# Kernel tuning notes

Hardware: AMD Instinct MI355X
Metric: run time of the kernel (lower is better)

The kernel has to match this reference:

```python
import jax, jax.numpy as jnp
import numpy as np

B, E, H, DEPTH = 8192, 512, 512, 1


def setup_inputs() -> dict:
    key = jax.random.key(0)
    ks = jax.random.split(key, 10)
    inp = {
        "X": jax.random.normal(ks[0], (B, E), jnp.float32),
        "prev_a": jax.random.normal(ks[1], (B, DEPTH + 1, H), jnp.float32),
        "prev_b": jax.random.normal(ks[2], (B, DEPTH + 1, H), jnp.float32),
        "prev_depth": jax.random.randint(ks[3], (B, 1), 0, DEPTH + 1, jnp.int32),
        # torch.nn.Linear weights, shape [out, in], y = x @ W.T
        "w_f": jax.random.normal(ks[4], (1, H), jnp.float32) * 0.02,
        "w_a00": jax.random.normal(ks[5], (H, E + H), jnp.float32) * 0.02,
        "w_a10": jax.random.normal(ks[6], (H, E + H), jnp.float32) * 0.02,
        "w_b00": jax.random.normal(ks[7], (H, E + 2 * H), jnp.float32) * 0.02,
        "w_b11": jax.random.normal(ks[8], (H, E + H), jnp.float32) * 0.02,
        "w_b10": jax.random.normal(ks[9], (H, E + H), jnp.float32) * 0.02,
    }
    return inp


def reference(X, prev_a, prev_b, prev_depth, w_f, w_a00, w_a10, w_b00, w_b11, w_b10):
    dt = X.dtype
    # gather prev_b at current depth per batch row: prev_b[b, prev_depth[b,0], :]
    b_top = jnp.take_along_axis(prev_b, prev_depth[:, :, None], axis=1)[:, 0, :]  # [B,H]
    # fork decision; torch rounds then casts to long -> no grad flows through w_f
    f_raw = jax.lax.stop_gradient(jnp.round(jax.nn.sigmoid(b_top @ w_f.T)))  # [B,1]
    all_zero = jnp.all(prev_depth == 0)
    f = jnp.where(all_zero, jnp.ones_like(f_raw), f_raw)
    j = jnp.where(all_zero, jnp.zeros_like(f_raw), f_raw)  # else-branch sets j = f
    next_depth = prev_depth + (f - j).astype(prev_depth.dtype)  # [B,1]

    d = 1  # depth fixed to 1
    pa, pb0, pb1 = prev_a[:, d, :], prev_b[:, d - 1, :], prev_b[:, d, :]

    fj, nn_, fn = f * j, (1.0 - f) * (1.0 - j), f * (1.0 - j)  # [B,1] gates
    eq = (next_depth == d).astype(dt)
    lt = (next_depth < d).astype(dt)

    nofork_nojoin_a = jnp.concatenate([X, pa], 1) @ w_a00.T
    fork_nojoin_a = jnp.concatenate([X, pb0], 1) @ w_a10.T
    next_a1 = eq * (fj * pa + nn_ * nofork_nojoin_a + fn * fork_nojoin_a) + lt * pa

    fork_join_b = jnp.concatenate([X, pb1], 1) @ w_b11.T
    nofork_nojoin_b = jnp.concatenate([X, pa, next_a1], 1) @ w_b00.T
    fork_nojoin_b = jnp.concatenate([X, next_a1], 1) @ w_b10.T
    next_b1 = eq * (fj * fork_join_b + nn_ * nofork_nojoin_b + fn * fork_nojoin_b) + lt * pb1

    zeros = jnp.zeros_like(next_a1)
    next_a = jnp.stack([zeros, next_a1], 1)  # [B, 2, H]
    next_b = jnp.stack([zeros, next_b1], 1)  # [B, 2, H]
    return next_a, next_b, next_depth, f, j
```

## Files before the change

kernel.cpp:

```cpp
#include <hip/hip_runtime.h>
#include <hip/hip_bf16.h>

typedef __attribute__((ext_vector_type(8))) __bf16 bf16x8;
typedef __attribute__((ext_vector_type(4))) float f32x4;
typedef __attribute__((ext_vector_type(4))) unsigned short u16x4;
typedef unsigned short u16;
typedef unsigned long long u64;

typedef __attribute__((address_space(1))) void gvoid;
typedef __attribute__((address_space(3))) void lvoid;

#define B_DIM 8192
#define MFMA(a, b, c) __builtin_amdgcn_mfma_f32_16x16x32_bf16((a), (b), (c), 0, 0, 0)

__device__ __forceinline__ u16x4 cvt4(f32x4 v) {
    u16x4 r;
    r.x = __builtin_bit_cast(u16, __float2bfloat16(v.x));
    r.y = __builtin_bit_cast(u16, __float2bfloat16(v.y));
    r.z = __builtin_bit_cast(u16, __float2bfloat16(v.z));
    r.w = __builtin_bit_cast(u16, __float2bfloat16(v.w));
    return r;
}

__device__ __forceinline__ void stage64(const u16* g, int ldg, u16* ls, int t) {
#pragma unroll
    for (int it = 0; it < 2; ++it) {
        int e = it * 2048 + t * 8;
        int r = e >> 6;
        int slot = (e & 63) >> 3;
        int csrc = (slot ^ (r & 7)) << 3;
        __builtin_amdgcn_global_load_lds((gvoid*)(g + (size_t)r * ldg + csrc),
                                         (lvoid*)&ls[e], 16, 0, 0);
    }
}

__device__ __forceinline__ bf16x8 ld_frag(const u16* ls, int row, int kslot) {
    return *(const bf16x8*)&ls[row * 64 + ((kslot ^ (row & 7)) << 3)];
}

__global__ void k_pre(const float* __restrict__ X, const float* __restrict__ prev_a,
                      const float* __restrict__ prev_b, const int* __restrict__ prev_depth,
                      const float* __restrict__ w_f,
                      const float* __restrict__ wa00f, const float* __restrict__ wa10f,
                      const float* __restrict__ wb00f, const float* __restrict__ wb11f,
                      const float* __restrict__ wb10f,
                      u16* __restrict__ Xb, u16* __restrict__ pab,
                      u16* __restrict__ pb0b, u16* __restrict__ pb1b,
                      u16* __restrict__ wa00b, u16* __restrict__ wa10b,
                      u16* __restrict__ wb00b, u16* __restrict__ wb11b,
                      u16* __restrict__ wb10b,
                      float* __restrict__ dotv,
                      float* __restrict__ outA, float* __restrict__ outB) {
    int blk = blockIdx.x;
    if (blk >= 2048) {
        int t = (blk - 2048) * 256 + threadIdx.x;
        const int S = 131072, SB = 196608;
        const float* src; u16* dst; int off;
        if      (t < S)            { src = wa00f; dst = wa00b; off = t; }
        else if (t < 2 * S)        { src = wa10f; dst = wa10b; off = t - S; }
        else if (t < 2 * S + SB)   { src = wb00f; dst = wb00b; off = t - 2 * S; }
        else if (t < 3 * S + SB)   { src = wb11f; dst = wb11b; off = t - 2 * S - SB; }
        else if (t < 4 * S + SB)   { src = wb10f; dst = wb10b; off = t - 3 * S - SB; }
        else return;
        f32x4 v = *(const f32x4*)(src + (size_t)off * 4);
        *(u16x4*)(dst + (size_t)off * 4) = cvt4(v);
        return;
    }
    int wv = threadIdx.x >> 6, l = threadIdx.x & 63;
    int row = blk * 4 + wv;
    size_t r512 = (size_t)row * 512, r1024 = (size_t)row * 1024;
    const int i1 = l * 4;
    const int i2 = 256 + l * 4;
    f32x4 x0  = *(const f32x4*)(X + r512 + i1);
    f32x4 x1  = *(const f32x4*)(X + r512 + i2);
    f32x4 pa0 = *(const f32x4*)(prev_a + r1024 + 512 + i1);
    f32x4 pa1 = *(const f32x4*)(prev_a + r1024 + 512 + i2);
    f32x4 q00 = *(const f32x4*)(prev_b + r1024 + i1);
    f32x4 q01 = *(const f32x4*)(prev_b + r1024 + i2);
    f32x4 q10 = *(const f32x4*)(prev_b + r1024 + 512 + i1);
    f32x4 q11 = *(const f32x4*)(prev_b + r1024 + 512 + i2);
    f32x4 w0  = *(const f32x4*)(w_f + i1);
    f32x4 w1  = *(const f32x4*)(w_f + i2);
    int depth = prev_depth[row];
    f32x4 b0 = depth ? q10 : q00;
    f32x4 b1 = depth ? q11 : q01;
    float dot = b0.x*w0.x + b0.y*w0.y + b0.z*w0.z + b0.w*w0.w
              + b1.x*w1.x + b1.y*w1.y + b1.z*w1.z + b1.w*w1.w;
    for (int off = 32; off > 0; off >>= 1) dot += __shfl_xor(dot, off, 64);

    *(u16x4*)(Xb   + r512 + i1) = cvt4(x0);
    *(u16x4*)(Xb   + r512 + i2) = cvt4(x1);
    *(u16x4*)(pab  + r512 + i1) = cvt4(pa0);
    *(u16x4*)(pab  + r512 + i2) = cvt4(pa1);
    *(u16x4*)(pb0b + r512 + i1) = cvt4(q00);
    *(u16x4*)(pb0b + r512 + i2) = cvt4(q01);
    *(u16x4*)(pb1b + r512 + i1) = cvt4(q10);
    *(u16x4*)(pb1b + r512 + i2) = cvt4(q11);
    f32x4 z; z.x = 0.f; z.y = 0.f; z.z = 0.f; z.w = 0.f;
    *(f32x4*)(outA + r1024 + i1) = z;
    *(f32x4*)(outA + r1024 + i2) = z;
    *(f32x4*)(outB + r1024 + i1) = z;
    *(f32x4*)(outB + r1024 + i2) = z;
    if (l == 0) dotv[row] = dot;
}

__global__ __launch_bounds__(1024) void k_scan(
        const float* __restrict__ dotv, const int* __restrict__ prev_depth,
        int* __restrict__ info, int* __restrict__ idx, int* __restrict__ cnt) {
    __shared__ u64 wtot[16];
    __shared__ int wany[16];
    const int tid = threadIdx.x, lane = tid & 63, wv = tid >> 6;
    int r0 = tid * 8;
    int dep[8]; float dv[8];
    int any = 0;
#pragma unroll
    for (int r = 0; r < 8; ++r) {
        dep[r] = prev_depth[r0 + r];
        dv[r] = dotv[r0 + r];
        any |= dep[r];
    }
    for (int off = 32; off > 0; off >>= 1) any |= __shfl_xor(any, off, 64);
    if (lane == 0) wany[wv] = any;
    __syncthreads();
    int ga = 0;
#pragma unroll
    for (int w = 0; w < 16; ++w) ga |= wany[w];
    int az = (ga == 0);

    int rcls[8], rf[8], rj[8], rnd[8];
    u64 pk = 0;
#pragma unroll
    for (int r = 0; r < 8; ++r) {
        float sg = 1.0f / (1.0f + expf(-dv[r]));
        int fi = (int)rintf(sg);
        int f = az ? 1 : fi;
        int j = az ? 0 : fi;
        int nd = dep[r] + f - j;
        int cls;
        if (nd == 1)     cls = f ? (j ? 2 : 1) : 0;
        else             cls = (nd < 1) ? 3 : 4;
        rcls[r] = cls; rf[r] = f; rj[r] = j; rnd[r] = nd;
        if (cls < 3) pk += 1ull << (cls * 21);
    }
    u64 own = pk;
    for (int off = 1; off < 64; off <<= 1) {
        u64 v = __shfl_up(pk, off, 64);
        if (lane >= off) pk += v;
    }
    if (lane == 63) wtot[wv] = pk;
    __syncthreads();
    u64 wbase = 0, tot = 0;
#pragma unroll
    for (int w = 0; w < 16; ++w) {
        u64 v = wtot[w];
        if (w < wv) wbase += v;
        tot += v;
    }
    u64 excl = wbase + pk - own;
    const u64 M21 = (1ull << 21) - 1;
    int tot0 = (int)(tot & M21), tot1 = (int)((tot >> 21) & M21), tot2 = (int)((tot >> 42) & M21);
    int base0 = 0;
    int base1 = (tot0 + 63) & ~63;
    int base2 = base1 + ((tot1 + 63) & ~63);
    int o0 = base0 + (int)(excl & M21);
    int o1 = base1 + (int)((excl >> 21) & M21);
    int o2 = base2 + (int)((excl >> 42) & M21);
#pragma unroll
    for (int r = 0; r < 8; ++r) {
        int row = r0 + r, cls = rcls[r], pos = 0;
        if (cls == 0)      { pos = o0++; idx[pos] = row; }
        else if (cls == 1) { pos = o1++; idx[pos] = row; }
        else if (cls == 2) { pos = o2++; idx[pos] = row; }
        info[row] = cls | (rf[r] << 3) | (rj[r] << 4) | (rnd[r] << 5) | (pos << 7);
    }
    if (tid < 64) {
        int p0 = tot0 + tid;          if (p0 < base1) idx[p0] = 0;
        int p1 = base1 + tot1 + tid;  if (p1 < base2) idx[p1] = 0;
        int end2 = base2 + ((tot2 + 63) & ~63);
        int p2 = base2 + tot2 + tid;  if (p2 < end2) idx[p2] = 0;
    }
    if (tid == 0) {
        cnt[0] = tot0; cnt[1] = tot1; cnt[2] = tot2;
        cnt[4] = base0; cnt[5] = base1; cnt[6] = base2;
    }
}

__global__ __launch_bounds__(256, 4) void k_s1x(
    const u16* __restrict__ Xb, const u16* __restrict__ pab,
    const u16* __restrict__ pb0b, const u16* __restrict__ pb1b,
    const u16* __restrict__ wa00, const u16* __restrict__ wa10,
    const u16* __restrict__ wb00, const u16* __restrict__ wb11,
    const u16* __restrict__ wb10,
    const int* __restrict__ idx, const int* __restrict__ cnt, const int* __restrict__ info,
    const float* __restrict__ prev_a, const float* __restrict__ prev_b,
    u16* __restrict__ na1_all, float* __restrict__ part,
    float* __restrict__ outA, float* __restrict__ outB,
    float* __restrict__ outD, float* __restrict__ outF, float* __restrict__ outJ)
{
    __shared__ u16 lsA[4096], lsB0[4096], lsB1[4096];
    int blk = (int)blockIdx.x;
    if (blk >= 1040) {
        int pb_ = blk - 1040;
        int wv = threadIdx.x >> 6, l = threadIdx.x & 63;
        int row = pb_ * 4 + wv;
        int inf = info[row];
        int cls = inf & 7;
        size_t r1024 = (size_t)row * 1024;
        const int i1 = l * 4, i2 = 256 + l * 4;
        if (l == 0) {
            outD[row] = (float)((inf >> 5) & 3);
            outF[row] = (float)((inf >> 3) & 1);
            outJ[row] = (float)((inf >> 4) & 1);
        }
        if (cls == 2 || cls == 3) {
            f32x4 pa0 = *(const f32x4*)(prev_a + r1024 + 512 + i1);
            f32x4 pa1 = *(const f32x4*)(prev_a + r1024 + 512 + i2);
            *(f32x4*)(outA + r1024 + 512 + i1) = pa0;
            *(f32x4*)(outA + r1024 + 512 + i2) = pa1;
            if (cls == 3) {
                f32x4 q10 = *(const f32x4*)(prev_b + r1024 + 512 + i1);
                f32x4 q11 = *(const f32x4*)(prev_b + r1024 + 512 + i2);
                *(f32x4*)(outB + r1024 + 512 + i1) = q10;
                *(f32x4*)(outB + r1024 + 512 + i2) = q11;
            }
        } else if (cls == 4) {
            f32x4 z; z.x = 0.f; z.y = 0.f; z.z = 0.f; z.w = 0.f;
            *(f32x4*)(outA + r1024 + 512 + i1) = z;
            *(f32x4*)(outA + r1024 + 512 + i2) = z;
            *(f32x4*)(outB + r1024 + 512 + i1) = z;
            *(f32x4*)(outB + r1024 + 512 + i2) = z;
        }
        return;
    }
    int c0 = cnt[0], c1 = cnt[1], c2 = cnt[2];
    int base0 = cnt[4], base1 = cnt[5], base2 = cnt[6];
    int t0 = (c0 + 63) >> 6, t1 = (c1 + 63) >> 6, t2 = (c2 + 63) >> 6;
    int T = blk >> 3, nt = blk & 7;
    int cls, mb, cc;
    const u16 *W0, *W1 = nullptr, *S2;
    int ldW1 = 0;
    if (T < t0)                { cls = 0; mb = base0 + T * 64; cc = c0; W0 = wa00; W1 = wb00; ldW1 = 1536; S2 = pab; }
    else if (T < t0 + t1)      { T -= t0; cls = 1; mb = base1 + T * 64; cc = c1; W0 = wa10; W1 = wb10; ldW1 = 1024; S2 = pb0b; }
    else if (T < t0 + t1 + t2) { T -= t0 + t1; cls = 2; mb = base2 + T * 64; cc = c2; W0 = wb11; S2 = pb1b; }
    else return;
    const int t = threadIdx.x;
    const int n0 = nt * 64;
    const int lane = t & 63, wv = t >> 6;
    const int wr = (wv >> 1) * 32, wc = (wv & 1) * 32;
    const int fr = lane & 15, fq = lane >> 4;

    int ri0 = idx[mb + (t >> 3)];
    int ri1 = idx[mb + 32 + (t >> 3)];
    const u16* xg0 = Xb + (size_t)ri0 * 512;
    const u16* xg1 = Xb + (size_t)ri1 * 512;
    const u16* sg0 = S2 + (size_t)ri0 * 512;
    const u16* sg1 = S2 + (size_t)ri1 * 512;
    const int csrc = ((t & 7) ^ ((t >> 3) & 7)) << 3;

    f32x4 acc0[2][2] = {}, acc1[2][2] = {};

    for (int kq = 0; kq < 16; ++kq) {
        int cb = (kq & 7) * 64;
        const u16* a0 = (kq < 8) ? xg0 : sg0;
        const u16* a1 = (kq < 8) ? xg1 : sg1;
        __builtin_amdgcn_global_load_lds((gvoid*)(a0 + cb + csrc), (lvoid*)&lsA[t * 8], 16, 0, 0);
        __builtin_amdgcn_global_load_lds((gvoid*)(a1 + cb + csrc), (lvoid*)&lsA[2048 + t * 8], 16, 0, 0);
        stage64(W0 + (size_t)n0 * 1024 + kq * 64, 1024, lsB0, t);
        bool dual = (cls == 0) || (cls == 1 && kq < 8);
        if (dual) stage64(W1 + (size_t)n0 * ldW1 + kq * 64, ldW1, lsB1, t);
        __syncthreads();
#pragma unroll
        for (int kk = 0; kk < 2; ++kk) {
            int ks = kk * 4 + fq;
            bf16x8 a[2], b0[2], b1[2];
#pragma unroll
            for (int mi = 0; mi < 2; ++mi) a[mi] = ld_frag(lsA, wr + mi * 16 + fr, ks);
#pragma unroll
            for (int ni = 0; ni < 2; ++ni) b0[ni] = ld_frag(lsB0, wc + ni * 16 + fr, ks);
            if (dual) {
#pragma unroll
                for (int ni = 0; ni < 2; ++ni) b1[ni] = ld_frag(lsB1, wc + ni * 16 + fr, ks);
            }
#pragma unroll
            for (int mi = 0; mi < 2; ++mi)
#pragma unroll
                for (int ni = 0; ni < 2; ++ni) {
                    acc0[mi][ni] = MFMA(a[mi], b0[ni], acc0[mi][ni]);
                    if (dual) acc1[mi][ni] = MFMA(a[mi], b1[ni], acc1[mi][ni]);
                }
        }
        __syncthreads();
    }
    int lt0 = T * 64;
#pragma unroll
    for (int mi = 0; mi < 2; ++mi)
#pragma unroll
        for (int jj = 0; jj < 4; ++jj) {
            int lr = wr + mi * 16 + fq * 4 + jj;
            if (lt0 + lr >= cc) continue;
            int grow = idx[mb + lr];
#pragma unroll
            for (int ni = 0; ni < 2; ++ni) {
                int col = n0 + wc + ni * 16 + fr;
                float v = acc0[mi][ni][jj];
                if (cls < 2) {
                    na1_all[(size_t)(mb + lr) * 512 + col] = __builtin_bit_cast(u16, __float2bfloat16(v));
                    outA[(size_t)grow * 1024 + 512 + col] = v;
                    part[(size_t)(mb + lr) * 512 + col] = acc1[mi][ni][jj];
                } else {
                    outB[(size_t)grow * 1024 + 512 + col] = v;
                }
            }
        }
}

__global__ __launch_bounds__(256, 4) void k_s2(
    const u16* __restrict__ na1_all,
    const u16* __restrict__ wb00, const u16* __restrict__ wb10,
    const int* __restrict__ idx, const int* __restrict__ cnt,
    const float* __restrict__ part, float* __restrict__ outB)
{
    __shared__ u16 lsA[4096], lsB[4096];
    int c0 = cnt[0], c1 = cnt[1];
    int base0 = cnt[4], base1 = cnt[5];
    int t0 = (c0 + 63) >> 6, t1 = (c1 + 63) >> 6;
    int blk = (int)blockIdx.x;
    int T = blk >> 3, nt = blk & 7;
    int mb, cc, ldW, kofs;
    const u16* W;
    if (T < t0)           { mb = base0 + T * 64; cc = c0; W = wb00; ldW = 1536; kofs = 1024; }
    else if (T < t0 + t1) { T -= t0; mb = base1 + T * 64; cc = c1; W = wb10; ldW = 1024; kofs = 512; }
    else return;
    const int t = threadIdx.x;
    const int n0 = nt * 64;
    const int lane = t & 63, wv = t >> 6;
    const int wr = (wv >> 1) * 32, wc = (wv & 1) * 32;
    const int fr = lane & 15, fq = lane >> 4;

    f32x4 acc[2][2];
#pragma unroll
    for (int mi = 0; mi < 2; ++mi)
#pragma unroll
        for (int ni = 0; ni < 2; ++ni)
#pragma unroll
            for (int jj = 0; jj < 4; ++jj)
                acc[mi][ni][jj] = part[(size_t)(mb + wr + mi * 16 + fq * 4 + jj) * 512
                                       + n0 + wc + ni * 16 + fr];

    for (int kq = 0; kq < 8; ++kq) {
        stage64(na1_all + (size_t)mb * 512 + kq * 64, 512, lsA, t);
        stage64(W + (size_t)n0 * ldW + kofs + kq * 64, ldW, lsB, t);
        __syncthreads();
#pragma unroll
        for (int kk = 0; kk < 2; ++kk) {
            int ks = kk * 4 + fq;
            bf16x8 a[2], b[2];
#pragma unroll
            for (int mi = 0; mi < 2; ++mi) a[mi] = ld_frag(lsA, wr + mi * 16 + fr, ks);
#pragma unroll
            for (int ni = 0; ni < 2; ++ni) b[ni] = ld_frag(lsB, wc + ni * 16 + fr, ks);
#pragma unroll
            for (int mi = 0; mi < 2; ++mi)
#pragma unroll
                for (int ni = 0; ni < 2; ++ni)
                    acc[mi][ni] = MFMA(a[mi], b[ni], acc[mi][ni]);
        }
        __syncthreads();
    }
    int lt0 = T * 64;
#pragma unroll
    for (int mi = 0; mi < 2; ++mi)
#pragma unroll
        for (int jj = 0; jj < 4; ++jj) {
            int lr = wr + mi * 16 + fq * 4 + jj;
            if (lt0 + lr >= cc) continue;
            int grow = idx[mb + lr];
#pragma unroll
            for (int ni = 0; ni < 2; ++ni) {
                int col = n0 + wc + ni * 16 + fr;
                outB[(size_t)grow * 1024 + 512 + col] = acc[mi][ni][jj];
            }
        }
}

extern "C" void kernel_launch(void* const* d_in, const int* in_sizes, int n_in,
                              void* d_out, int out_size, void* d_ws, size_t ws_size,
                              hipStream_t stream) {
    const float* X          = (const float*)d_in[0];
    const float* prev_a     = (const float*)d_in[1];
    const float* prev_b     = (const float*)d_in[2];
    const int*   prev_depth = (const int*)d_in[3];
    const float* w_f        = (const float*)d_in[4];
    const float* w_a00      = (const float*)d_in[5];
    const float* w_a10      = (const float*)d_in[6];
    const float* w_b00      = (const float*)d_in[7];
    const float* w_b11      = (const float*)d_in[8];
    const float* w_b10      = (const float*)d_in[9];

    float* out  = (float*)d_out;
    float* outA = out;
    float* outB = out + 8388608;
    float* outD = out + 16777216;
    float* outF = outD + 8192;
    float* outJ = outF + 8192;

    char* ws = (char*)d_ws;
    size_t off = 0;
    auto alloc = [&](size_t bytes) -> char* {
        char* p = ws + off;
        off += (bytes + 255) & ~(size_t)255;
        return p;
    };
    const int ROWS = 8448;
    u16* Xb     = (u16*)alloc((size_t)B_DIM * 512 * 2);
    u16* pab    = (u16*)alloc((size_t)B_DIM * 512 * 2);
    u16* pb0b   = (u16*)alloc((size_t)B_DIM * 512 * 2);
    u16* pb1b   = (u16*)alloc((size_t)B_DIM * 512 * 2);
    u16* na1_all = (u16*)alloc((size_t)ROWS * 512 * 2);
    float* part  = (float*)alloc((size_t)ROWS * 512 * 4);
    u16* wa00b = (u16*)alloc((size_t)512 * 1024 * 2);
    u16* wa10b = (u16*)alloc((size_t)512 * 1024 * 2);
    u16* wb00b = (u16*)alloc((size_t)512 * 1536 * 2);
    u16* wb11b = (u16*)alloc((size_t)512 * 1024 * 2);
    u16* wb10b = (u16*)alloc((size_t)512 * 1024 * 2);
    float* dotv = (float*)alloc((size_t)B_DIM * 4);
    int* info   = (int*)alloc((size_t)B_DIM * 4);
    int* idx    = (int*)alloc((size_t)ROWS * 4);
    int* cnt    = (int*)alloc(256);
    if (off > ws_size) return;

    k_pre<<<4864, 256, 0, stream>>>(X, prev_a, prev_b, prev_depth, w_f,
                                    w_a00, w_a10, w_b00, w_b11, w_b10,
                                    Xb, pab, pb0b, pb1b,
                                    wa00b, wa10b, wb00b, wb11b, wb10b,
                                    dotv, outA, outB);
    k_scan<<<1, 1024, 0, stream>>>(dotv, prev_depth, info, idx, cnt);
    k_s1x<<<3088, 256, 0, stream>>>(Xb, pab, pb0b, pb1b,
                                    wa00b, wa10b, wb00b, wb11b, wb10b,
                                    idx, cnt, info, prev_a, prev_b,
                                    na1_all, part, outA, outB, outD, outF, outJ);
    k_s2<<<1040, 256, 0, stream>>>(na1_all, wb00b, wb10b, idx, cnt, part, outB);
}
```

Baseline: 68.23 us.

## Gather class-sorted bf16 activation rows after scan instead of converting all inputs upfront

The pre-kernel now only computes the fork dot products from the depth-selected prev_b row and converts the weights. Previously it converted X, pa, pb0 and pb1 for every row. A new mid kernel runs after the scan. It gathers each row's X and its one class-specific second operand into a contiguous, class-sorted bf16 buffer, and it also does the output zeroing and passthrough copies. The GEMM kernel then stages its A tiles with plain contiguous loads instead of indexed row gathers, and it no longer carries the passthrough blocks. This cuts the bf16 conversion traffic and simplifies the GEMM loads, at the cost of one extra kernel launch and a serial dependence between the gather and the GEMM.

```diff
diff --git a/kernel.cpp b/kernel.cpp
--- a/kernel.cpp
+++ b/kernel.cpp
@@ -38,19 +38,15 @@
     return *(const bf16x8*)&ls[row * 64 + ((kslot ^ (row & 7)) << 3)];
 }
 
-__global__ void k_pre(const float* __restrict__ X, const float* __restrict__ prev_a,
-                      const float* __restrict__ prev_b, const int* __restrict__ prev_depth,
-                      const float* __restrict__ w_f,
-                      const float* __restrict__ wa00f, const float* __restrict__ wa10f,
-                      const float* __restrict__ wb00f, const float* __restrict__ wb11f,
-                      const float* __restrict__ wb10f,
-                      u16* __restrict__ Xb, u16* __restrict__ pab,
-                      u16* __restrict__ pb0b, u16* __restrict__ pb1b,
-                      u16* __restrict__ wa00b, u16* __restrict__ wa10b,
-                      u16* __restrict__ wb00b, u16* __restrict__ wb11b,
-                      u16* __restrict__ wb10b,
-                      float* __restrict__ dotv,
-                      float* __restrict__ outA, float* __restrict__ outB) {
+__global__ void k_dots(const float* __restrict__ prev_b, const int* __restrict__ prev_depth,
+                       const float* __restrict__ w_f,
+                       const float* __restrict__ wa00f, const float* __restrict__ wa10f,
+                       const float* __restrict__ wb00f, const float* __restrict__ wb11f,
+                       const float* __restrict__ wb10f,
+                       u16* __restrict__ wa00b, u16* __restrict__ wa10b,
+                       u16* __restrict__ wb00b, u16* __restrict__ wb11b,
+                       u16* __restrict__ wb10b,
+                       float* __restrict__ dotv) {
     int blk = blockIdx.x;
     if (blk >= 2048) {
         int t = (blk - 2048) * 256 + threadIdx.x;
@@ -68,39 +64,16 @@
     }
     int wv = threadIdx.x >> 6, l = threadIdx.x & 63;
     int row = blk * 4 + wv;
-    size_t r512 = (size_t)row * 512, r1024 = (size_t)row * 1024;
-    const int i1 = l * 4;
-    const int i2 = 256 + l * 4;
-    f32x4 x0  = *(const f32x4*)(X + r512 + i1);
-    f32x4 x1  = *(const f32x4*)(X + r512 + i2);
-    f32x4 pa0 = *(const f32x4*)(prev_a + r1024 + 512 + i1);
-    f32x4 pa1 = *(const f32x4*)(prev_a + r1024 + 512 + i2);
-    f32x4 q00 = *(const f32x4*)(prev_b + r1024 + i1);
-    f32x4 q01 = *(const f32x4*)(prev_b + r1024 + i2);
-    f32x4 q10 = *(const f32x4*)(prev_b + r1024 + 512 + i1);
-    f32x4 q11 = *(const f32x4*)(prev_b + r1024 + 512 + i2);
-    f32x4 w0  = *(const f32x4*)(w_f + i1);
-    f32x4 w1  = *(const f32x4*)(w_f + i2);
     int depth = prev_depth[row];
-    f32x4 b0 = depth ? q10 : q00;
-    f32x4 b1 = depth ? q11 : q01;
-    float dot = b0.x*w0.x + b0.y*w0.y + b0.z*w0.z + b0.w*w0.w
-              + b1.x*w1.x + b1.y*w1.y + b1.z*w1.z + b1.w*w1.w;
+    const float* bt = prev_b + (size_t)row * 1024 + (size_t)depth * 512;
+    const int i1 = l * 4, i2 = 256 + l * 4;
+    f32x4 v0 = *(const f32x4*)(bt + i1);
+    f32x4 v1 = *(const f32x4*)(bt + i2);
+    f32x4 w0 = *(const f32x4*)(w_f + i1);
+    f32x4 w1 = *(const f32x4*)(w_f + i2);
+    float dot = v0.x*w0.x + v0.y*w0.y + v0.z*w0.z + v0.w*w0.w
+              + v1.x*w1.x + v1.y*w1.y + v1.z*w1.z + v1.w*w1.w;
     for (int off = 32; off > 0; off >>= 1) dot += __shfl_xor(dot, off, 64);
-
-    *(u16x4*)(Xb   + r512 + i1) = cvt4(x0);
-    *(u16x4*)(Xb   + r512 + i2) = cvt4(x1);
-    *(u16x4*)(pab  + r512 + i1) = cvt4(pa0);
-    *(u16x4*)(pab  + r512 + i2) = cvt4(pa1);
-    *(u16x4*)(pb0b + r512 + i1) = cvt4(q00);
-    *(u16x4*)(pb0b + r512 + i2) = cvt4(q01);
-    *(u16x4*)(pb1b + r512 + i1) = cvt4(q10);
-    *(u16x4*)(pb1b + r512 + i2) = cvt4(q11);
-    f32x4 z; z.x = 0.f; z.y = 0.f; z.z = 0.f; z.w = 0.f;
-    *(f32x4*)(outA + r1024 + i1) = z;
-    *(f32x4*)(outA + r1024 + i2) = z;
-    *(f32x4*)(outB + r1024 + i1) = z;
-    *(f32x4*)(outB + r1024 + i2) = z;
     if (l == 0) dotv[row] = dot;
 }
 
@@ -185,63 +158,92 @@
     }
 }
 
-__global__ __launch_bounds__(256, 4) void k_s1x(
-    const u16* __restrict__ Xb, const u16* __restrict__ pab,
-    const u16* __restrict__ pb0b, const u16* __restrict__ pb1b,
+__global__ void k_mid(const float* __restrict__ X, const float* __restrict__ prev_a,
+                      const float* __restrict__ prev_b,
+                      const int* __restrict__ info, const int* __restrict__ idx,
+                      const int* __restrict__ cnt,
+                      u16* __restrict__ A_all,
+                      float* __restrict__ outA, float* __restrict__ outB,
+                      float* __restrict__ outD, float* __restrict__ outF,
+                      float* __restrict__ outJ) {
+    int blk = (int)blockIdx.x;
+    int wv = threadIdx.x >> 6, l = threadIdx.x & 63;
+    const int i1 = l * 4, i2 = 256 + l * 4;
+    if (blk >= 2048) {
+        int p = (blk - 2048) * 4 + wv;
+        int base1 = cnt[5], base2 = cnt[6];
+        int end2 = base2 + ((cnt[2] + 63) & ~63);
+        if (p >= end2) return;
+        const float* sec = (p < base1) ? (prev_a + 512)
+                         : (p < base2) ? prev_b
+                                       : (prev_b + 512);
+        int row = idx[p];
+        size_t r512 = (size_t)row * 512, r1024 = (size_t)row * 1024;
+        f32x4 xa = *(const f32x4*)(X + r512 + i1);
+        f32x4 xb = *(const f32x4*)(X + r512 + i2);
+        f32x4 sa = *(const f32x4*)(sec + r1024 + i1);
+        f32x4 sb = *(const f32x4*)(sec + r1024 + i2);
+        size_t pbase = (size_t)p * 1024;
+        *(u16x4*)(A_all + pbase + i1)       = cvt4(xa);
+        *(u16x4*)(A_all + pbase + i2)       = cvt4(xb);
+        *(u16x4*)(A_all + pbase + 512 + i1) = cvt4(sa);
+        *(u16x4*)(A_all + pbase + 512 + i2) = cvt4(sb);
+        return;
+    }
+    int row = blk * 4 + wv;
+    int inf = info[row];
+    int cls = inf & 7;
+    size_t r1024 = (size_t)row * 1024;
+    f32x4 z; z.x = 0.f; z.y = 0.f; z.z = 0.f; z.w = 0.f;
+    *(f32x4*)(outA + r1024 + i1) = z;
+    *(f32x4*)(outA + r1024 + i2) = z;
+    *(f32x4*)(outB + r1024 + i1) = z;
+    *(f32x4*)(outB + r1024 + i2) = z;
+    if (l == 0) {
+        outD[row] = (float)((inf >> 5) & 3);
+        outF[row] = (float)((inf >> 3) & 1);
+        outJ[row] = (float)((inf >> 4) & 1);
+    }
+    if (cls == 2 || cls == 3) {
+        f32x4 pa0 = *(const f32x4*)(prev_a + r1024 + 512 + i1);
+        f32x4 pa1 = *(const f32x4*)(prev_a + r1024 + 512 + i2);
+        *(f32x4*)(outA + r1024 + 512 + i1) = pa0;
+        *(f32x4*)(outA + r1024 + 512 + i2) = pa1;
+        if (cls == 3) {
+            f32x4 q10 = *(const f32x4*)(prev_b + r1024 + 512 + i1);
+            f32x4 q11 = *(const f32x4*)(prev_b + r1024 + 512 + i2);
+            *(f32x4*)(outB + r1024 + 512 + i1) = q10;
+            *(f32x4*)(outB + r1024 + 512 + i2) = q11;
+        }
+    } else if (cls == 4) {
+        *(f32x4*)(outA + r1024 + 512 + i1) = z;
+        *(f32x4*)(outA + r1024 + 512 + i2) = z;
+        *(f32x4*)(outB + r1024 + 512 + i1) = z;
+        *(f32x4*)(outB + r1024 + 512 + i2) = z;
+    }
+}
+
+__global__ __launch_bounds__(256, 4) void k_s1(
+    const u16* __restrict__ A_all,
     const u16* __restrict__ wa00, const u16* __restrict__ wa10,
     const u16* __restrict__ wb00, const u16* __restrict__ wb11,
     const u16* __restrict__ wb10,
-    const int* __restrict__ idx, const int* __restrict__ cnt, const int* __restrict__ info,
-    const float* __restrict__ prev_a, const float* __restrict__ prev_b,
+    const int* __restrict__ idx, const int* __restrict__ cnt,
     u16* __restrict__ na1_all, float* __restrict__ part,
-    float* __restrict__ outA, float* __restrict__ outB,
-    float* __restrict__ outD, float* __restrict__ outF, float* __restrict__ outJ)
+    float* __restrict__ outA, float* __restrict__ outB)
 {
     __shared__ u16 lsA[4096], lsB0[4096], lsB1[4096];
-    int blk = (int)blockIdx.x;
-    if (blk >= 1040) {
-        int pb_ = blk - 1040;
-        int wv = threadIdx.x >> 6, l = threadIdx.x & 63;
-        int row = pb_ * 4 + wv;
-        int inf = info[row];
-        int cls = inf & 7;
-        size_t r1024 = (size_t)row * 1024;
-        const int i1 = l * 4, i2 = 256 + l * 4;
-        if (l == 0) {
-            outD[row] = (float)((inf >> 5) & 3);
-            outF[row] = (float)((inf >> 3) & 1);
-            outJ[row] = (float)((inf >> 4) & 1);
-        }
-        if (cls == 2 || cls == 3) {
-            f32x4 pa0 = *(const f32x4*)(prev_a + r1024 + 512 + i1);
-            f32x4 pa1 = *(const f32x4*)(prev_a + r1024 + 512 + i2);
-            *(f32x4*)(outA + r1024 + 512 + i1) = pa0;
-            *(f32x4*)(outA + r1024 + 512 + i2) = pa1;
-            if (cls == 3) {
-                f32x4 q10 = *(const f32x4*)(prev_b + r1024 + 512 + i1);
-                f32x4 q11 = *(const f32x4*)(prev_b + r1024 + 512 + i2);
-                *(f32x4*)(outB + r1024 + 512 + i1) = q10;
-                *(f32x4*)(outB + r1024 + 512 + i2) = q11;
-            }
-        } else if (cls == 4) {
-            f32x4 z; z.x = 0.f; z.y = 0.f; z.z = 0.f; z.w = 0.f;
-            *(f32x4*)(outA + r1024 + 512 + i1) = z;
-            *(f32x4*)(outA + r1024 + 512 + i2) = z;
-            *(f32x4*)(outB + r1024 + 512 + i1) = z;
-            *(f32x4*)(outB + r1024 + 512 + i2) = z;
-        }
-        return;
-    }
     int c0 = cnt[0], c1 = cnt[1], c2 = cnt[2];
     int base0 = cnt[4], base1 = cnt[5], base2 = cnt[6];
     int t0 = (c0 + 63) >> 6, t1 = (c1 + 63) >> 6, t2 = (c2 + 63) >> 6;
+    int blk = (int)blockIdx.x;
     int T = blk >> 3, nt = blk & 7;
     int cls, mb, cc;
-    const u16 *W0, *W1 = nullptr, *S2;
+    const u16 *W0, *W1 = nullptr;
     int ldW1 = 0;
-    if (T < t0)                { cls = 0; mb = base0 + T * 64; cc = c0; W0 = wa00; W1 = wb00; ldW1 = 1536; S2 = pab; }
-    else if (T < t0 + t1)      { T -= t0; cls = 1; mb = base1 + T * 64; cc = c1; W0 = wa10; W1 = wb10; ldW1 = 1024; S2 = pb0b; }
-    else if (T < t0 + t1 + t2) { T -= t0 + t1; cls = 2; mb = base2 + T * 64; cc = c2; W0 = wb11; S2 = pb1b; }
+    if (T < t0)                { cls = 0; mb = base0 + T * 64; cc = c0; W0 = wa00; W1 = wb00; ldW1 = 1536; }
+    else if (T < t0 + t1)      { T -= t0; cls = 1; mb = base1 + T * 64; cc = c1; W0 = wa10; W1 = wb10; ldW1 = 1024; }
+    else if (T < t0 + t1 + t2) { T -= t0 + t1; cls = 2; mb = base2 + T * 64; cc = c2; W0 = wb11; }
     else return;
     const int t = threadIdx.x;
     const int n0 = nt * 64;
@@ -249,25 +251,14 @@
     const int wr = (wv >> 1) * 32, wc = (wv & 1) * 32;
     const int fr = lane & 15, fq = lane >> 4;
 
-    int ri0 = idx[mb + (t >> 3)];
-    int ri1 = idx[mb + 32 + (t >> 3)];
-    const u16* xg0 = Xb + (size_t)ri0 * 512;
-    const u16* xg1 = Xb + (size_t)ri1 * 512;
-    const u16* sg0 = S2 + (size_t)ri0 * 512;
-    const u16* sg1 = S2 + (size_t)ri1 * 512;
-    const int csrc = ((t & 7) ^ ((t >> 3) & 7)) << 3;
-
     f32x4 acc0[2][2] = {}, acc1[2][2] = {};
 
     for (int kq = 0; kq < 16; ++kq) {
-        int cb = (kq & 7) * 64;
-        const u16* a0 = (kq < 8) ? xg0 : sg0;
-        const u16* a1 = (kq < 8) ? xg1 : sg1;
-        __builtin_amdgcn_global_load_lds((gvoid*)(a0 + cb + csrc), (lvoid*)&lsA[t * 8], 16, 0, 0);
-        __builtin_amdgcn_global_load_lds((gvoid*)(a1 + cb + csrc), (lvoid*)&lsA[2048 + t * 8], 16, 0, 0);
-        stage64(W0 + (size_t)n0 * 1024 + kq * 64, 1024, lsB0, t);
+        int cb = kq * 64;
+        stage64(A_all + (size_t)mb * 1024 + cb, 1024, lsA, t);
+        stage64(W0 + (size_t)n0 * 1024 + cb, 1024, lsB0, t);
         bool dual = (cls == 0) || (cls == 1 && kq < 8);
-        if (dual) stage64(W1 + (size_t)n0 * ldW1 + kq * 64, ldW1, lsB1, t);
+        if (dual) stage64(W1 + (size_t)n0 * ldW1 + cb, ldW1, lsB1, t);
         __syncthreads();
 #pragma unroll
         for (int kk = 0; kk < 2; ++kk) {
@@ -412,12 +403,9 @@
         return p;
     };
     const int ROWS = 8448;
-    u16* Xb     = (u16*)alloc((size_t)B_DIM * 512 * 2);
-    u16* pab    = (u16*)alloc((size_t)B_DIM * 512 * 2);
-    u16* pb0b   = (u16*)alloc((size_t)B_DIM * 512 * 2);
-    u16* pb1b   = (u16*)alloc((size_t)B_DIM * 512 * 2);
-    u16* na1_all = (u16*)alloc((size_t)ROWS * 512 * 2);
-    float* part  = (float*)alloc((size_t)ROWS * 512 * 4);
+    u16* A_all    = (u16*)alloc((size_t)ROWS * 1024 * 2);
+    u16* na1_all  = (u16*)alloc((size_t)ROWS * 512 * 2);
+    float* part   = (float*)alloc((size_t)ROWS * 512 * 4);
     u16* wa00b = (u16*)alloc((size_t)512 * 1024 * 2);
     u16* wa10b = (u16*)alloc((size_t)512 * 1024 * 2);
     u16* wb00b = (u16*)alloc((size_t)512 * 1536 * 2);
@@ -429,15 +417,13 @@
     int* cnt    = (int*)alloc(256);
     if (off > ws_size) return;
 
-    k_pre<<<4864, 256, 0, stream>>>(X, prev_a, prev_b, prev_depth, w_f,
-                                    w_a00, w_a10, w_b00, w_b11, w_b10,
-                                    Xb, pab, pb0b, pb1b,
-                                    wa00b, wa10b, wb00b, wb11b, wb10b,
-                                    dotv, outA, outB);
+    k_dots<<<4864, 256, 0, stream>>>(prev_b, prev_depth, w_f,
+                                     w_a00, w_a10, w_b00, w_b11, w_b10,
+                                     wa00b, wa10b, wb00b, wb11b, wb10b, dotv);
     k_scan<<<1, 1024, 0, stream>>>(dotv, prev_depth, info, idx, cnt);
-    k_s1x<<<3088, 256, 0, stream>>>(Xb, pab, pb0b, pb1b,
-                                    wa00b, wa10b, wb00b, wb11b, wb10b,
-                                    idx, cnt, info, prev_a, prev_b,
-                                    na1_all, part, outA, outB, outD, outF, outJ);
+    k_mid<<<4128, 256, 0, stream>>>(X, prev_a, prev_b, info, idx, cnt,
+                                    A_all, outA, outB, outD, outF, outJ);
+    k_s1<<<1040, 256, 0, stream>>>(A_all, wa00b, wa10b, wb00b, wb11b, wb10b,
+                                   idx, cnt, na1_all, part, outA, outB);
     k_s2<<<1040, 256, 0, stream>>>(na1_all, wb00b, wb10b, idx, cnt, part, outB);
 }
```

Measured after the change: 65.73 us. 3.7% less time.
